# Kernel optimization log

Hardware: AMD Instinct MI355X
Metric: run time of the kernel (lower is better)

Reference implementation:

```python
import jax, jax.numpy as jnp
import numpy as np

GAMMA = 0.5
K = 3
SKIP_THRESHOLD = 1.0


def setup_inputs() -> dict:
    key = jax.random.key(0)
    ks = jax.random.split(key, 11)
    in_dim, out_dim, mem_len = 1024, 128, 131072
    inp = {
        "x": jax.random.normal(ks[0], (1, in_dim), jnp.float32),
        "mean": jax.random.normal(ks[1], (in_dim,), jnp.float32),
        "std": jax.random.uniform(ks[2], (in_dim,), jnp.float32, 0.5, 1.5),
        "memory": jax.random.normal(ks[3], (mem_len, out_dim), jnp.float32),
        "mem_data": jax.random.normal(ks[4], (mem_len, in_dim), jnp.float32),
        "W_enc": jax.random.normal(ks[5], (in_dim, out_dim), jnp.float32) * 0.02,
        "b_enc": jnp.zeros((out_dim,), jnp.float32),
        "W_dec": jax.random.normal(ks[6], (out_dim, in_dim), jnp.float32) * 0.02,
        "b_dec": jnp.zeros((in_dim,), jnp.float32),
        "win_mean": jnp.zeros((), jnp.float32),   # WindowLoss running mean
        "win_std": jnp.ones((), jnp.float32),     # WindowLoss sample std (1 if population_std==0)
    }
    return inp


def reference(x, mean, std, memory, mem_data, W_enc, b_enc, W_dec, b_dec, win_mean, win_std):
    # normalize: new = (x - mean) / std, zero where std == 0
    new = jnp.where(std == 0, 0.0, (x - mean) / std)            # [1, in_dim]
    # encoder: Linear + Tanh
    enc = jnp.tanh(new @ W_enc + b_enc)                          # [1, out_dim]
    # window_loss: decoder reconstruction MSE, gated by ndtr of z-scored loss
    rec = enc @ W_dec + b_dec                                    # [1, in_dim]
    mse = jnp.mean((rec - new) ** 2)                             # scalar
    prob = jax.scipy.special.ndtr((mse - win_mean) / win_std)    # torch uses loss.item() -> constant
    win_loss = (SKIP_THRESHOLD - prob) / SKIP_THRESHOLD * mse
    # L1-distance top-k (smallest) against the memory bank
    dist = jnp.sum(jnp.abs(memory - enc), axis=1)                # [mem_len]
    neg_d, idx = jax.lax.top_k(-dist, K)
    distances = -neg_d                                           # [K] smallest distances
    expw = GAMMA ** jnp.arange(K, dtype=jnp.float32)
    loss_values = jnp.sum(distances * expw) / jnp.sum(expw)
    # conditional FIFO scatter update at the nearest index
    cond = loss_values <= win_loss
    i0 = idx[0]
    new_memory = jnp.where(cond, memory.at[i0].set(enc[0]), memory)
    new_mem_data = jnp.where(cond, mem_data.at[i0].set(x[0]), mem_data)
    loss_combined = win_loss + loss_values
    return loss_combined, new_memory, new_mem_data
```

## Files before the change

kernel.cpp:

```cpp
#include <hip/hip_runtime.h>
#include <math.h>
#include <float.h>

#define IN_DIM   1024
#define OUT_DIM  128
#define MEM_LEN  131072
#define COPY_GRID 8192
#define DIST_BLOCKS 2048

#define NA_FLOATS  ((long long)MEM_LEN * OUT_DIM)
#define NB_FLOATS  ((long long)MEM_LEN * IN_DIM)
#define N_TOTAL    (NA_FLOATS + NB_FLOATS)
#define NA_CHUNKS  (NA_FLOATS / 4)
#define CMAX       ((N_TOTAL - 4) / 4)

__device__ __forceinline__ void ins3(float v, int i,
    float& v0, int& i0, float& v1, int& i1, float& v2, int& i2) {
  if (v < v0 || (v == v0 && i < i0)) {
    v2 = v1; i2 = i1; v1 = v0; i1 = i0; v0 = v; i0 = i;
  } else if (v < v1 || (v == v1 && i < i1)) {
    v2 = v1; i2 = i1; v1 = v; i1 = i;
  } else if (v < v2 || (v == v2 && i < i2)) {
    v2 = v; i2 = i;
  }
}

__global__ __launch_bounds__(1024) void k1_encode(
    const float* __restrict__ x, const float* __restrict__ mean,
    const float* __restrict__ stdv, const float* __restrict__ W_enc,
    const float* __restrict__ b_enc, const float* __restrict__ W_dec,
    const float* __restrict__ b_dec, const float* __restrict__ win_mean,
    const float* __restrict__ win_std,
    float* __restrict__ ws_enc, float* __restrict__ ws_winloss) {
  __shared__ float s_new[IN_DIM];
  __shared__ float s_part[8][OUT_DIM];
  __shared__ float s_enc[OUT_DIM];
  __shared__ float s_red[16];
  const int t = threadIdx.x;
  const float sd = stdv[t];
  const float nv = (sd == 0.0f) ? 0.0f : (x[t] - mean[t]) / sd;
  s_new[t] = nv;
  __syncthreads();
  const int o = t & (OUT_DIM - 1);
  const int p = t >> 7;
  float partial = 0.0f;
  #pragma unroll 8
  for (int i = 0; i < 128; ++i) {
    const int k = p * 128 + i;
    partial += s_new[k] * W_enc[k * OUT_DIM + o];
  }
  s_part[p][o] = partial;
  __syncthreads();
  if (t < OUT_DIM) {
    float sum = b_enc[t];
    #pragma unroll
    for (int pp = 0; pp < 8; ++pp) sum += s_part[pp][t];
    const float e = tanhf(sum);
    s_enc[t] = e;
    ws_enc[t] = e;
  }
  __syncthreads();
  float r = b_dec[t];
  #pragma unroll 8
  for (int k = 0; k < OUT_DIM; ++k) r += s_enc[k] * W_dec[k * IN_DIM + t];
  const float diff = r - nv;
  float sq = diff * diff;
  for (int off = 32; off; off >>= 1) sq += __shfl_xor(sq, off, 64);
  const int lane = t & 63, wid = t >> 6;
  if (lane == 0) s_red[wid] = sq;
  __syncthreads();
  if (t == 0) {
    float tot = 0.0f;
    #pragma unroll
    for (int w = 0; w < 16; ++w) tot += s_red[w];
    const float mse = tot / (float)IN_DIM;
    const float z = (mse - win_mean[0]) / win_std[0];
    const float prob = 0.5f * erfcf(-z * 0.70710678118654752440f);
    ws_winloss[0] = (1.0f - prob) * mse;
  }
}

__global__ __launch_bounds__(256) void k2_dist(
    const float* __restrict__ memory, const float* __restrict__ ws_enc,
    float* __restrict__ topv, int* __restrict__ topi) {
  const int t = threadIdx.x;
  const int lane = t & 63;
  const int wid = t >> 6;
  const int half = lane >> 5;
  const int col  = lane & 31;
  const float4 e = reinterpret_cast<const float4*>(ws_enc)[col];
  const float4* m4 = reinterpret_cast<const float4*>(memory);
  float v0 = FLT_MAX, v1 = FLT_MAX, v2 = FLT_MAX;
  int i0 = 0x7fffffff, i1 = 0x7fffffff, i2 = 0x7fffffff;
  const int r0 = (blockIdx.x * 4 + wid) * 16;
  for (int rr = 0; rr < 16; rr += 2) {
    const float4 m = m4[(size_t)(r0 + rr) * 32 + lane];
    float d = fabsf(m.x - e.x) + fabsf(m.y - e.y)
            + fabsf(m.z - e.z) + fabsf(m.w - e.w);
    d += __shfl_xor(d, 1, 64);
    d += __shfl_xor(d, 2, 64);
    d += __shfl_xor(d, 4, 64);
    d += __shfl_xor(d, 8, 64);
    d += __shfl_xor(d, 16, 64);
    ins3(d, r0 + rr + half, v0, i0, v1, i1, v2, i2);
  }
  {
    const float w0 = __shfl_xor(v0, 32, 64);
    const float w1 = __shfl_xor(v1, 32, 64);
    const float w2 = __shfl_xor(v2, 32, 64);
    const int j0 = __shfl_xor(i0, 32, 64);
    const int j1 = __shfl_xor(i1, 32, 64);
    const int j2 = __shfl_xor(i2, 32, 64);
    ins3(w0, j0, v0, i0, v1, i1, v2, i2);
    ins3(w1, j1, v0, i0, v1, i1, v2, i2);
    ins3(w2, j2, v0, i0, v1, i1, v2, i2);
  }
  __shared__ float sv[4][3];
  __shared__ int   si[4][3];
  if (lane == 0) {
    sv[wid][0] = v0; sv[wid][1] = v1; sv[wid][2] = v2;
    si[wid][0] = i0; si[wid][1] = i1; si[wid][2] = i2;
  }
  __syncthreads();
  if (t == 0) {
    for (int w = 1; w < 4; ++w)
      for (int j = 0; j < 3; ++j)
        ins3(sv[w][j], si[w][j], v0, i0, v1, i1, v2, i2);
    topv[blockIdx.x * 3 + 0] = v0; topi[blockIdx.x * 3 + 0] = i0;
    topv[blockIdx.x * 3 + 1] = v1; topi[blockIdx.x * 3 + 1] = i1;
    topv[blockIdx.x * 3 + 2] = v2; topi[blockIdx.x * 3 + 2] = i2;
  }
}

__global__ __launch_bounds__(256) void copy_all(
    const float* __restrict__ memory, const float* __restrict__ mem_data,
    float* __restrict__ out) {
  float4* out4 = reinterpret_cast<float4*>(out);
  const long long stride = (long long)gridDim.x * 256;
  long long c = (long long)blockIdx.x * 256 + threadIdx.x + 1;
  #pragma unroll 4
  for (; c <= CMAX; c += stride) {
    float4 v;
    if (__builtin_expect(c == NA_CHUNKS, 0)) {
      v.x = memory[NA_FLOATS - 1];
      v.y = mem_data[0]; v.z = mem_data[1]; v.w = mem_data[2];
    } else {
      const long long s = 4 * c - 1;
      const float* src = (s >= NA_FLOATS) ? (mem_data + (s - NA_FLOATS))
                                          : (memory + s);
      __builtin_memcpy(&v, src, 16);
    }
    out4[c] = v;
  }
  if (blockIdx.x == 0 && threadIdx.x == 0) {
    out[1] = memory[0]; out[2] = memory[1]; out[3] = memory[2];
    out[N_TOTAL] = mem_data[NB_FLOATS - 1];
  }
}

__global__ __launch_bounds__(1024) void k3_topk_update(
    const float* __restrict__ topv, const int* __restrict__ topi,
    const float* __restrict__ ws_winloss, const float* __restrict__ ws_enc,
    const float* __restrict__ x, float* __restrict__ out_loss,
    float* __restrict__ out_mem, float* __restrict__ out_md) {
  const int t = threadIdx.x;
  const int n = DIST_BLOCKS * 3;
  float v0 = FLT_MAX, v1 = FLT_MAX, v2 = FLT_MAX;
  int i0 = 0x7fffffff, i1 = 0x7fffffff, i2 = 0x7fffffff;
  for (int j = t; j < n; j += 1024) ins3(topv[j], topi[j], v0, i0, v1, i1, v2, i2);
  for (int off = 32; off; off >>= 1) {
    const float ov0 = __shfl_xor(v0, off, 64);
    const float ov1 = __shfl_xor(v1, off, 64);
    const float ov2 = __shfl_xor(v2, off, 64);
    const int oi0 = __shfl_xor(i0, off, 64);
    const int oi1 = __shfl_xor(i1, off, 64);
    const int oi2 = __shfl_xor(i2, off, 64);
    ins3(ov0, oi0, v0, i0, v1, i1, v2, i2);
    ins3(ov1, oi1, v0, i0, v1, i1, v2, i2);
    ins3(ov2, oi2, v0, i0, v1, i1, v2, i2);
  }
  __shared__ float sv[16][3];
  __shared__ int   si[16][3];
  __shared__ int s_i0, s_cond;
  const int lane = t & 63, wid = t >> 6;
  if (lane == 0) {
    sv[wid][0] = v0; sv[wid][1] = v1; sv[wid][2] = v2;
    si[wid][0] = i0; si[wid][1] = i1; si[wid][2] = i2;
  }
  __syncthreads();
  if (t == 0) {
    for (int w = 1; w < 16; ++w)
      for (int j = 0; j < 3; ++j)
        ins3(sv[w][j], si[w][j], v0, i0, v1, i1, v2, i2);
    const float loss_values = (v0 + 0.5f * v1 + 0.25f * v2) / 1.75f;
    const float wl = ws_winloss[0];
    out_loss[0] = wl + loss_values;
    s_i0 = i0;
    s_cond = (loss_values <= wl) ? 1 : 0;
  }
  __syncthreads();
  if (s_cond) {
    if (t < OUT_DIM) out_mem[(size_t)s_i0 * OUT_DIM + t] = ws_enc[t];
    out_md[(size_t)s_i0 * IN_DIM + t] = x[t];
  }
}

extern "C" void kernel_launch(void* const* d_in, const int* in_sizes, int n_in,
                              void* d_out, int out_size, void* d_ws, size_t ws_size,
                              hipStream_t stream) {
  const float* x        = (const float*)d_in[0];
  const float* mean     = (const float*)d_in[1];
  const float* stdv     = (const float*)d_in[2];
  const float* memory   = (const float*)d_in[3];
  const float* mem_data = (const float*)d_in[4];
  const float* W_enc    = (const float*)d_in[5];
  const float* b_enc    = (const float*)d_in[6];
  const float* W_dec    = (const float*)d_in[7];
  const float* b_dec    = (const float*)d_in[8];
  const float* win_mean = (const float*)d_in[9];
  const float* win_std  = (const float*)d_in[10];

  float* out      = (float*)d_out;
  float* out_loss = out;
  float* out_mem  = out + 1;
  float* out_md   = out + 1 + (size_t)MEM_LEN * OUT_DIM;

  float* ws        = (float*)d_ws;
  float* ws_enc    = ws;
  float* ws_wl     = ws + 128;
  float* ws_topv   = ws + 256;
  int*   ws_topi   = (int*)(ws + 256 + DIST_BLOCKS * 3);

  k1_encode<<<1, 1024, 0, stream>>>(x, mean, stdv, W_enc, b_enc, W_dec, b_dec,
                                    win_mean, win_std, ws_enc, ws_wl);
  k2_dist<<<DIST_BLOCKS, 256, 0, stream>>>(memory, ws_enc, ws_topv, ws_topi);
  copy_all<<<COPY_GRID, 256, 0, stream>>>(memory, mem_data, out);
  k3_topk_update<<<1, 1024, 0, stream>>>(ws_topv, ws_topi, ws_wl, ws_enc, x,
                                         out_loss, out_mem, out_md);
}
```

Baseline: 369.3 us.

## Use aligned vector loads with wave shuffles for offset-by-one output copy

The copy kernel previously read unaligned 16-byte chunks, since the output is offset by one float. It now has each wave load four aligned float4s per 1024-float frame and rebuild the shifted layout with lane shuffles, reading one scalar edge value per frame. The grid shrinks so each wave handles frames in a grid-stride loop. This aims to turn misaligned global loads into aligned ones, at the cost of extra shuffles and one scalar load per frame.

```diff
diff --git a/kernel.cpp b/kernel.cpp
--- a/kernel.cpp
+++ b/kernel.cpp
@@ -5,14 +5,14 @@
 #define IN_DIM   1024
 #define OUT_DIM  128
 #define MEM_LEN  131072
-#define COPY_GRID 8192
+#define COPY_GRID 2048
 #define DIST_BLOCKS 2048
 
 #define NA_FLOATS  ((long long)MEM_LEN * OUT_DIM)
 #define NB_FLOATS  ((long long)MEM_LEN * IN_DIM)
 #define N_TOTAL    (NA_FLOATS + NB_FLOATS)
-#define NA_CHUNKS  (NA_FLOATS / 4)
-#define CMAX       ((N_TOTAL - 4) / 4)
+#define NFRAMES    (N_TOTAL / 1024)
+#define FRAME_MEM  16384
 
 __device__ __forceinline__ void ins3(float v, int i,
     float& v0, int& i0, float& v1, int& i1, float& v2, int& i2) {
@@ -135,27 +135,41 @@
 __global__ __launch_bounds__(256) void copy_all(
     const float* __restrict__ memory, const float* __restrict__ mem_data,
     float* __restrict__ out) {
+  const int t = threadIdx.x;
+  const int lane = t & 63;
+  const int wid  = t >> 6;
+  const float4* mem4 = reinterpret_cast<const float4*>(memory);
+  const float4* md4  = reinterpret_cast<const float4*>(mem_data);
   float4* out4 = reinterpret_cast<float4*>(out);
-  const long long stride = (long long)gridDim.x * 256;
-  long long c = (long long)blockIdx.x * 256 + threadIdx.x + 1;
-  #pragma unroll 4
-  for (; c <= CMAX; c += stride) {
-    float4 v;
-    if (__builtin_expect(c == NA_CHUNKS, 0)) {
-      v.x = memory[NA_FLOATS - 1];
-      v.y = mem_data[0]; v.z = mem_data[1]; v.w = mem_data[2];
-    } else {
-      const long long s = 4 * c - 1;
-      const float* src = (s >= NA_FLOATS) ? (mem_data + (s - NA_FLOATS))
-                                          : (memory + s);
-      __builtin_memcpy(&v, src, 16);
+  const long long wstride = (long long)gridDim.x * 4;
+  for (long long s = (long long)blockIdx.x * 4 + wid; s < NFRAMES; s += wstride) {
+    const float4* src4 = (s < FRAME_MEM) ? (mem4 + (s << 8))
+                                         : (md4 + ((s - FRAME_MEM) << 8));
+    float edge = 0.0f;
+    if (s > 0) {
+      const long long sd = (s << 10) - 1;
+      edge = (sd < NA_FLOATS) ? memory[sd] : mem_data[sd - NA_FLOATS];
     }
-    out4[c] = v;
-  }
-  if (blockIdx.x == 0 && threadIdx.x == 0) {
-    out[1] = memory[0]; out[2] = memory[1]; out[3] = memory[2];
+    const float4 a0 = src4[lane];
+    const float4 a1 = src4[lane + 64];
+    const float4 a2 = src4[lane + 128];
+    const float4 a3 = src4[lane + 192];
+    float p0 = __shfl_up(a0.w, 1, 64);
+    float p1 = __shfl_up(a1.w, 1, 64);
+    float p2 = __shfl_up(a2.w, 1, 64);
+    float p3 = __shfl_up(a3.w, 1, 64);
+    const float t1 = __shfl(a0.w, 63, 64);
+    const float t2 = __shfl(a1.w, 63, 64);
+    const float t3 = __shfl(a2.w, 63, 64);
+    if (lane == 0) { p0 = edge; p1 = t1; p2 = t2; p3 = t3; }
+    float4* ob = out4 + (s << 8);
+    ob[lane]       = make_float4(p0, a0.x, a0.y, a0.z);
+    ob[lane + 64]  = make_float4(p1, a1.x, a1.y, a1.z);
+    ob[lane + 128] = make_float4(p2, a2.x, a2.y, a2.z);
+    ob[lane + 192] = make_float4(p3, a3.x, a3.y, a3.z);
+  }
+  if (blockIdx.x == 0 && t == 0)
     out[N_TOTAL] = mem_data[NB_FLOATS - 1];
-  }
 }
 
 __global__ __launch_bounds__(1024) void k3_topk_update(
```

Result: faster. 327.8 us (-11.2%).
